# Kernel optimization log

Hardware: AMD Instinct MI355X
Metric: run time of the kernel (lower is better)

Reference implementation:

```python
import jax, jax.numpy as jnp
import numpy as np

B, S, H1, H2, D4, LAT, DD1, DD2, K = 8192, 4096, 196, 10, 1024, 32, 1024, 2048, 21

def _knn_mask(rng, rows, cols, k):
    # disjoint-group style mask: each column has exactly k ones (as produced by knnLayer's non-overlap grouping)
    m = np.zeros((rows, cols), dtype=np.float32)
    order = np.argsort(rng.random((rows, cols)), axis=0)[:k]  # [k, cols]
    m[order, np.arange(cols)[None, :]] = 1.0
    return m

def _glorot(rng, shape):
    lim = np.sqrt(6.0 / (shape[0] + shape[1]))
    return (rng.uniform(-lim, lim, size=shape)).astype(np.float32)

def setup_inputs() -> dict:
    rng = np.random.default_rng(0)
    key = jax.random.key(0)
    x = jax.random.uniform(key, (B, S), dtype=jnp.float32)
    inp = {
        'x': x,
        'C1': jnp.asarray(_knn_mask(rng, S, H1, K)),
        'W1': jnp.asarray(_glorot(rng, (S, H1))),
        'b1': jnp.zeros((H1,), jnp.float32),
        'C2': jnp.asarray(_knn_mask(rng, H1, H2, K)),
        'W2': jnp.asarray(_glorot(rng, (H1, H2))),
        'b2': jnp.zeros((H2,), jnp.float32),
        'W3': jnp.asarray(_glorot(rng, (H2, D4))),
        'b3': jnp.zeros((D4,), jnp.float32),
        'W4': jnp.asarray(_glorot(rng, (D4, LAT))),
        'b4': jnp.zeros((LAT,), jnp.float32),
        'Wd1': jnp.asarray(_glorot(rng, (LAT, DD1))),
        'bd1': jnp.zeros((DD1,), jnp.float32),
        'Wd2': jnp.asarray(_glorot(rng, (DD1, DD2))),
        'bd2': jnp.zeros((DD2,), jnp.float32),
        'Wd3': jnp.asarray(_glorot(rng, (DD2, S))),
        'bd3': jnp.zeros((S,), jnp.float32),
    }
    return inp

def reference(x, C1, W1, b1, C2, W2, b2, W3, b3, W4, b4, Wd1, bd1, Wd2, bd2, Wd3, bd3):
    # encoder: two masked (CustomConnected) layers + two dense layers
    h = jax.nn.relu(x @ (W1 * C1) + b1)            # [B, H1]
    h = jax.nn.relu(h @ (W2 * C2) + b2)            # [B, H2]
    h = jax.nn.relu(h @ W3 + b3)                    # [B, S/4]
    z = jax.nn.relu(h @ W4 + b4)                    # [B, latent]
    # decoder: relu, relu, sigmoid
    d = jax.nn.relu(z @ Wd1 + bd1)                  # [B, S/4]
    d = jax.nn.relu(d @ Wd2 + bd2)                  # [B, S/2]
    out = jax.nn.sigmoid(d @ Wd3 + bd3)             # [B, S]
    return out
```

## Files before the change

kernel.cpp:

```cpp
#include <hip/hip_runtime.h>
#include <hip/hip_fp8.h>
#include <cstdint>
#include <cstddef>

typedef __attribute__((ext_vector_type(4))) float f32x4;
typedef __attribute__((ext_vector_type(8))) int i32x8;

#define DEVINL __device__ __forceinline__

DEVINL unsigned short f2bf(float f){
  union { float f; unsigned u; } v; v.f = f;
  unsigned r = v.u + 0x7fffu + ((v.u >> 16) & 1u);
  return (unsigned short)(r >> 16);
}
DEVINL float bf2f(unsigned short h){
  union { unsigned u; float f; } v; v.u = ((unsigned)h) << 16;
  return v.f;
}
DEVINL unsigned char f2fp8(float f){
  __hip_fp8_e4m3 t(f);
  return (unsigned char)t.__x;
}
DEVINL void gload_lds16(const void* g, void* l){
  __builtin_amdgcn_global_load_lds((const __attribute__((address_space(1))) void*)g,
                                   (__attribute__((address_space(3))) void*)l, 16, 0, 0);
}

#define ACT_SCALE 64.0f
#define W_SCALE   16.0f
#define E8M0_ACT  121
#define E8M0_W    123

__global__ __launch_bounds__(256) void transpose_fp8(
    const float* __restrict__ W, unsigned char* __restrict__ Wt, int K, int N)
{
  __shared__ unsigned char tile[32][33];
  int k0 = blockIdx.x * 32, n0 = blockIdx.y * 32;
  int tx = threadIdx.x & 31, ty = threadIdx.x >> 5;
  #pragma unroll
  for (int i = 0; i < 4; ++i) {
    int k = k0 + ty + 8*i, n = n0 + tx;
    tile[ty + 8*i][tx] = f2fp8(W[(size_t)k*N + n] * W_SCALE);
  }
  __syncthreads();
  #pragma unroll
  for (int i = 0; i < 4; ++i) {
    int n = n0 + ty + 8*i, k = k0 + tx;
    Wt[(size_t)n*K + k] = tile[tx][ty + 8*i];
  }
}

__global__ __launch_bounds__(256) void build_sparse(
    const float* __restrict__ C1, const float* __restrict__ W1,
    unsigned* __restrict__ packed)
{
  const int j = blockIdx.x;
  const int w = threadIdx.x >> 6, l = threadIdx.x & 63;
  __shared__ int wcnt[4], wbase[4];
  int cnt = 0;
  #pragma unroll 4
  for (int it = 0; it < 16; ++it) {
    int k = w*1024 + it*64 + l;
    float c = C1[(size_t)k*196 + j];
    unsigned long long m = __ballot(c != 0.f);
    cnt += (int)__popcll(m);
  }
  if (l == 0) wcnt[w] = cnt;
  __syncthreads();
  if (threadIdx.x < 21) packed[j*21 + threadIdx.x] = 0;
  if (threadIdx.x == 0) {
    int b = 0;
    #pragma unroll
    for (int i = 0; i < 4; ++i) { wbase[i] = b; b += wcnt[i]; }
  }
  __syncthreads();
  int base = wbase[w];
  #pragma unroll 4
  for (int it = 0; it < 16; ++it) {
    int k = w*1024 + it*64 + l;
    float c = C1[(size_t)k*196 + j];
    unsigned long long m = __ballot(c != 0.f);
    if (c != 0.f) {
      int pos = base + (int)__popcll(m & ((1ull << l) - 1ull));
      if (pos < 21)
        packed[j*21 + pos] = ((unsigned)k << 16)
                           | (unsigned)f2bf(W1[(size_t)k*196 + j] * c);
    }
    base += (int)__popcll(m);
  }
}

__global__ __launch_bounds__(256) void layer1_sparse(
    const float* __restrict__ x, const unsigned* __restrict__ packed,
    const float* __restrict__ b1, unsigned short* __restrict__ h1)
{
  __shared__ float xs[2*4096];
  const int t = threadIdx.x;
  const long m0 = (long)blockIdx.x * 2;
  const float4* src = (const float4*)(x + m0*4096);
  #pragma unroll
  for (int i = 0; i < 8; ++i) ((float4*)xs)[t + i*256] = src[t + i*256];
  __syncthreads();
  for (int e = t; e < 2*196; e += 256) {
    int row = (e >= 196) ? 1 : 0;
    int col = e - row*196;
    const float* xr = xs + row*4096;
    float acc = b1[col];
    #pragma unroll
    for (int i = 0; i < 21; ++i) {
      unsigned p = packed[col*21 + i];
      acc += xr[p >> 16] * bf2f((unsigned short)(p & 0xffffu));
    }
    h1[(m0 + row)*256 + col] = f2bf(fmaxf(acc, 0.f));
  }
}

template<int ACT>
__global__ __launch_bounds__(256) void gemm_fp8(
    const unsigned char* __restrict__ A, const unsigned char* __restrict__ Bt,
    const float* __restrict__ bias, void* __restrict__ Cptr, int K, int ldC)
{
  constexpr int BM = 128, BN = 128, BK = 128;
  constexpr int HM = 64, HN = 64, FM = 4, FN = 4;
  __shared__ __align__(16) unsigned char smem[32768];
  unsigned char* As = smem;
  unsigned char* Bs = smem + 16384;
  const int tid  = threadIdx.x;
  const int lane = tid & 63;
  const int w    = tid >> 6;
  const int wm = w & 1, wn = w >> 1;
  const int q = lane >> 4, l16 = lane & 15;
  const long m0 = (long)blockIdx.x * BM;
  const long n0 = (long)blockIdx.y * BN;

  f32x4 acc[FM][FN] = {};

  for (int k0 = 0; k0 < K; k0 += BK) {
    #pragma unroll
    for (int it = 0; it < 4; ++it) {
      int seg = tid + it*256;
      int row = seg >> 3;
      int g   = (5*(seg & 7) + 3*row) & 7;
      gload_lds16(A + (m0 + row)*(long)K + k0 + g*16, As + seg*16);
    }
    #pragma unroll
    for (int it = 0; it < 4; ++it) {
      int seg = tid + it*256;
      int row = seg >> 3;
      int g   = (5*(seg & 7) + 3*row) & 7;
      gload_lds16(Bt + (n0 + row)*(long)K + k0 + g*16, Bs + seg*16);
    }
    __syncthreads();

    i32x8 a[FM], b[FN];
    #pragma unroll
    for (int i = 0; i < FM; ++i) {
      int r = wm*HM + i*16 + l16;
      const uint4* p = (const uint4*)(As + r*BK);
      int c0 = (2*q + r) & 7;
      union { uint4 v[2]; i32x8 f; } u;
      u.v[0] = p[c0];
      u.v[1] = p[(c0 + 5) & 7];
      a[i] = u.f;
    }
    #pragma unroll
    for (int j = 0; j < FN; ++j) {
      int r = wn*HN + j*16 + l16;
      const uint4* p = (const uint4*)(Bs + r*BK);
      int c0 = (2*q + r) & 7;
      union { uint4 v[2]; i32x8 f; } u;
      u.v[0] = p[c0];
      u.v[1] = p[(c0 + 5) & 7];
      b[j] = u.f;
    }
    #pragma unroll
    for (int i = 0; i < FM; ++i)
      #pragma unroll
      for (int j = 0; j < FN; ++j)
        acc[i][j] = __builtin_amdgcn_mfma_scale_f32_16x16x128_f8f6f4(
            a[i], b[j], acc[i][j], 0, 0, 0, E8M0_ACT, 0, E8M0_W);
    __syncthreads();
  }

  if constexpr (ACT == 0) {
    #pragma unroll
    for (int j = 0; j < FN; ++j) {
      int cl = wn*HN + j*16 + l16;
      float bv = bias[n0 + cl];
      #pragma unroll
      for (int i = 0; i < FM; ++i) {
        #pragma unroll
        for (int r = 0; r < 4; ++r) {
          int rl = wm*HM + i*16 + q*4 + r;
          smem[rl*144 + cl] = f2fp8(fmaxf(acc[i][j][r] + bv, 0.f) * ACT_SCALE);
        }
      }
    }
    __syncthreads();
    unsigned char* C = (unsigned char*)Cptr;
    #pragma unroll
    for (int it = 0; it < 4; ++it) {
      int seg = tid + it*256;
      int row = seg >> 3;
      *(uint4*)(C + (m0 + row)*(long)ldC + n0 + (seg & 7)*16) =
          *(const uint4*)(smem + row*144 + (seg & 7)*16);
    }
  } else {
    float* C = (float*)Cptr;
    #pragma unroll
    for (int j = 0; j < FN; ++j) {
      long col = n0 + wn*HN + j*16 + l16;
      float bv = bias[col];
      #pragma unroll
      for (int i = 0; i < FM; ++i) {
        #pragma unroll
        for (int r = 0; r < 4; ++r) {
          long row = m0 + wm*HM + i*16 + q*4 + r;
          float v = acc[i][j][r] + bv;
          C[row*(long)ldC + col] = 1.f / (1.f + __expf(-v));
        }
      }
    }
  }
}

__global__ __launch_bounds__(256) void layer2345(
    const unsigned short* __restrict__ h1,
    const float* __restrict__ W2, const float* __restrict__ C2, const float* __restrict__ b2,
    const float* __restrict__ W3, const float* __restrict__ b3,
    const float* __restrict__ W4, const float* __restrict__ b4,
    const float* __restrict__ Wd1, const float* __restrict__ bd1,
    unsigned char* __restrict__ d1)
{
  __shared__ float h1s[4][200];
  __shared__ float h2s[4][10];
  __shared__ float h3s[4][1024];
  __shared__ float part[8][128];
  __shared__ float zs[4][32];
  const int t = threadIdx.x;
  const int w = t >> 6, l = t & 63;
  const long m0 = (long)blockIdx.x * 4;

  for (int e = t; e < 4*196; e += 256) {
    int row = e / 196, col = e - row*196;
    h1s[row][col] = bf2f(h1[(m0 + row)*256 + col]);
  }
  __syncthreads();

  {
    float acc[10];
    #pragma unroll
    for (int n = 0; n < 10; ++n) acc[n] = 0.f;
    #pragma unroll
    for (int it = 0; it < 4; ++it) {
      int k = l + it*64;
      if (k < 196) {
        float a = h1s[w][k];
        #pragma unroll
        for (int n = 0; n < 10; ++n) acc[n] += a * W2[k*10 + n] * C2[k*10 + n];
      }
    }
    #pragma unroll
    for (int off = 32; off > 0; off >>= 1) {
      #pragma unroll
      for (int n = 0; n < 10; ++n) acc[n] += __shfl_down(acc[n], off, 64);
    }
    if (l < 10) h2s[w][l] = fmaxf(acc[l] + b2[l], 0.f);
  }
  __syncthreads();

  #pragma unroll
  for (int jj = 0; jj < 4; ++jj) {
    int n = w*256 + jj*64 + l;
    float a0 = b3[n], a1 = a0, a2 = a0, a3 = a0;
    #pragma unroll
    for (int k = 0; k < 10; ++k) {
      float wv = W3[k*1024 + n];
      a0 += h2s[0][k]*wv; a1 += h2s[1][k]*wv;
      a2 += h2s[2][k]*wv; a3 += h2s[3][k]*wv;
    }
    h3s[0][n] = fmaxf(a0, 0.f); h3s[1][n] = fmaxf(a1, 0.f);
    h3s[2][n] = fmaxf(a2, 0.f); h3s[3][n] = fmaxf(a3, 0.f);
  }
  __syncthreads();

  {
    int n = t & 31, kg = t >> 5;
    float a0 = 0.f, a1 = 0.f, a2 = 0.f, a3 = 0.f;
    for (int k = kg*128; k < kg*128 + 128; ++k) {
      float wv = W4[k*32 + n];
      a0 += h3s[0][k]*wv; a1 += h3s[1][k]*wv;
      a2 += h3s[2][k]*wv; a3 += h3s[3][k]*wv;
    }
    part[kg][0*32 + n] = a0; part[kg][1*32 + n] = a1;
    part[kg][2*32 + n] = a2; part[kg][3*32 + n] = a3;
  }
  __syncthreads();
  if (t < 128) {
    float s = 0.f;
    #pragma unroll
    for (int kg = 0; kg < 8; ++kg) s += part[kg][t];
    zs[t >> 5][t & 31] = fmaxf(s + b4[t & 31], 0.f);
  }
  __syncthreads();

  #pragma unroll
  for (int jj = 0; jj < 4; ++jj) {
    int n = w*256 + jj*64 + l;
    float a0 = bd1[n], a1 = a0, a2 = a0, a3 = a0;
    #pragma unroll
    for (int k = 0; k < 32; ++k) {
      float wv = Wd1[k*1024 + n];
      a0 += zs[0][k]*wv; a1 += zs[1][k]*wv;
      a2 += zs[2][k]*wv; a3 += zs[3][k]*wv;
    }
    d1[(m0 + 0)*1024 + n] = f2fp8(fmaxf(a0, 0.f) * ACT_SCALE);
    d1[(m0 + 1)*1024 + n] = f2fp8(fmaxf(a1, 0.f) * ACT_SCALE);
    d1[(m0 + 2)*1024 + n] = f2fp8(fmaxf(a2, 0.f) * ACT_SCALE);
    d1[(m0 + 3)*1024 + n] = f2fp8(fmaxf(a3, 0.f) * ACT_SCALE);
  }
}

extern "C" void kernel_launch(void* const* d_in, const int* in_sizes, int n_in,
                              void* d_out, int out_size, void* d_ws, size_t ws_size,
                              hipStream_t stream)
{
  (void)in_sizes; (void)n_in; (void)out_size; (void)ws_size;
  const float* x   = (const float*)d_in[0];
  const float* C1  = (const float*)d_in[1];
  const float* W1  = (const float*)d_in[2];
  const float* b1  = (const float*)d_in[3];
  const float* C2  = (const float*)d_in[4];
  const float* W2  = (const float*)d_in[5];
  const float* b2  = (const float*)d_in[6];
  const float* W3  = (const float*)d_in[7];
  const float* b3  = (const float*)d_in[8];
  const float* W4  = (const float*)d_in[9];
  const float* b4  = (const float*)d_in[10];
  const float* Wd1 = (const float*)d_in[11];
  const float* bd1 = (const float*)d_in[12];
  const float* Wd2 = (const float*)d_in[13];
  const float* bd2 = (const float*)d_in[14];
  const float* Wd3 = (const float*)d_in[15];
  const float* bd3 = (const float*)d_in[16];
  float* out = (float*)d_out;

  char* ws = (char*)d_ws;
  size_t off = 0;
  auto alloc = [&](size_t bytes) -> void* {
    void* p = ws + off; off += (bytes + 255) & ~(size_t)255; return p;
  };
  unsigned char* Wt2 = (unsigned char*)alloc((size_t)2048*1024);
  unsigned char* Wt3 = (unsigned char*)alloc((size_t)4096*2048);
  unsigned*      pk  = (unsigned*)     alloc((size_t)196*21*4);
  unsigned short* h1 = (unsigned short*)alloc((size_t)8192*256*2);
  unsigned char*  d1 = (unsigned char*) alloc((size_t)8192*1024);
  unsigned char*  d2 = (unsigned char*) alloc((size_t)8192*2048);

  build_sparse<<<dim3(196), 256, 0, stream>>>(C1, W1, pk);
  transpose_fp8<<<dim3(1024/32, 2048/32), 256, 0, stream>>>(Wd2, Wt2, 1024, 2048);
  transpose_fp8<<<dim3(2048/32, 4096/32), 256, 0, stream>>>(Wd3, Wt3, 2048, 4096);

  layer1_sparse<<<dim3(8192/2), 256, 0, stream>>>(x, pk, b1, h1);
  layer2345<<<dim3(8192/4), 256, 0, stream>>>(h1, W2, C2, b2, W3, b3, W4, b4,
                                              Wd1, bd1, d1);
  gemm_fp8<0><<<dim3(8192/128, 2048/128), 256, 0, stream>>>(
      d1, Wt2, bd2, d2, 1024, 2048);
  gemm_fp8<1><<<dim3(8192/128, 4096/128), 256, 0, stream>>>(
      d2, Wt3, bd3, out, 2048, 4096);
}
```

Before: 464.5 us.

## Rewrite FP8 GEMM as 256x256 double-buffered 8-wave kernel with phased prefetch

```diff
diff --git a/kernel.cpp b/kernel.cpp
--- a/kernel.cpp
+++ b/kernel.cpp
@@ -115,107 +115,174 @@
   }
 }
 
+
+#define MXMFMA(va, vb, c) __builtin_amdgcn_mfma_scale_f32_16x16x128_f8f6f4( \
+    (va), (vb), (c), 0, 0, 0, E8M0_ACT, 0, E8M0_W)
+
+#define MFMA8(I, va0, va1) \
+  acc[(I)][0]   = MXMFMA(va0, b0, acc[(I)][0]); \
+  acc[(I)][1]   = MXMFMA(va0, b1, acc[(I)][1]); \
+  acc[(I)][2]   = MXMFMA(va0, b2, acc[(I)][2]); \
+  acc[(I)][3]   = MXMFMA(va0, b3, acc[(I)][3]); \
+  acc[(I)+1][0] = MXMFMA(va1, b0, acc[(I)+1][0]); \
+  acc[(I)+1][1] = MXMFMA(va1, b1, acc[(I)+1][1]); \
+  acc[(I)+1][2] = MXMFMA(va1, b2, acc[(I)+1][2]); \
+  acc[(I)+1][3] = MXMFMA(va1, b3, acc[(I)+1][3]);
+
 template<int ACT>
-__global__ __launch_bounds__(256) void gemm_fp8(
+__global__ __launch_bounds__(512, 2) void gemm_fp8_8ph(
     const unsigned char* __restrict__ A, const unsigned char* __restrict__ Bt,
     const float* __restrict__ bias, void* __restrict__ Cptr, int K, int ldC)
 {
-  constexpr int BM = 128, BN = 128, BK = 128;
-  constexpr int HM = 64, HN = 64, FM = 4, FN = 4;
-  __shared__ __align__(16) unsigned char smem[32768];
-  unsigned char* As = smem;
-  unsigned char* Bs = smem + 16384;
+  constexpr int BM = 256, BN = 256;
+  extern __shared__ unsigned char sm[];
   const int tid  = threadIdx.x;
   const int lane = tid & 63;
   const int w    = tid >> 6;
-  const int wm = w & 1, wn = w >> 1;
+  const int wm = w >> 2, wn = w & 3;
   const int q = lane >> 4, l16 = lane & 15;
   const long m0 = (long)blockIdx.x * BM;
   const long n0 = (long)blockIdx.y * BN;
 
-  f32x4 acc[FM][FN] = {};
-
-  for (int k0 = 0; k0 < K; k0 += BK) {
-    #pragma unroll
-    for (int it = 0; it < 4; ++it) {
-      int seg = tid + it*256;
-      int row = seg >> 3;
-      int g   = (5*(seg & 7) + 3*row) & 7;
-      gload_lds16(A + (m0 + row)*(long)K + k0 + g*16, As + seg*16);
-    }
-    #pragma unroll
-    for (int it = 0; it < 4; ++it) {
-      int seg = tid + it*256;
-      int row = seg >> 3;
-      int g   = (5*(seg & 7) + 3*row) & 7;
-      gload_lds16(Bt + (n0 + row)*(long)K + k0 + g*16, Bs + seg*16);
-    }
+  unsigned char* Ac = sm;
+  unsigned char* Bc = sm + 32768;
+  unsigned char* An = sm + 65536;
+  unsigned char* Bn = sm + 98304;
+
+  f32x4 acc[8][4] = {};
+  const int NT = K >> 7;
+
+  auto stageA = [&](unsigned char* Ld, int qr, int kk) {
+    int seg  = qr*512 + tid;
+    int rblk = seg >> 7, ci = seg & 127;
+    int h = ci >> 6, rem = ci & 63;
+    int qq = rem >> 4, rloc = rem & 15;
+    int r = rblk*16 + rloc, c = qq*2 + h;
+    gload_lds16(A + (m0 + r)*(long)K + kk + c*16, Ld + seg*16);
+  };
+  auto stageB = [&](unsigned char* Ld, int qr, int kk) {
+    int seg  = qr*512 + tid;
+    int rblk = seg >> 7, ci = seg & 127;
+    int h = ci >> 6, rem = ci & 63;
+    int qq = rem >> 4, rloc = rem & 15;
+    int r = rblk*16 + rloc, c = qq*2 + h;
+    gload_lds16(Bt + (n0 + r)*(long)K + kk + c*16, Ld + seg*16);
+  };
+  auto rdfrag = [&](const unsigned char* Ld, int rblk) -> i32x8 {
+    union { uint4 v[2]; i32x8 f; } u;
+    const unsigned char* p = Ld + rblk*2048 + lane*16;
+    u.v[0] = *(const uint4*)p;
+    u.v[1] = *(const uint4*)(p + 1024);
+    return u.f;
+  };
+
+  #pragma unroll
+  for (int qr = 0; qr < 4; ++qr) stageA(Ac, qr, 0);
+  #pragma unroll
+  for (int qr = 0; qr < 4; ++qr) stageB(Bc, qr, 0);
+  asm volatile("s_waitcnt vmcnt(0)" ::: "memory");
+  __builtin_amdgcn_s_barrier();
+
+  for (int kt = 0; kt < NT; ++kt) {
+    const bool haveNext = (kt + 1 < NT);
+    const int kk = (kt + 1) << 7;
+    i32x8 b0, b1, b2, b3;
+
+    if (haveNext) { stageB(Bn, 0, kk); stageB(Bn, 1, kk); }
+    b0 = rdfrag(Bc, wn*4 + 0); b1 = rdfrag(Bc, wn*4 + 1);
+    b2 = rdfrag(Bc, wn*4 + 2); b3 = rdfrag(Bc, wn*4 + 3);
+    {
+      i32x8 a0 = rdfrag(Ac, wm*8 + 0), a1 = rdfrag(Ac, wm*8 + 1);
+      __builtin_amdgcn_s_barrier();
+      asm volatile("s_waitcnt lgkmcnt(0)" ::: "memory");
+      __builtin_amdgcn_sched_barrier(0);
+      __builtin_amdgcn_s_setprio(1);
+      MFMA8(0, a0, a1)
+      __builtin_amdgcn_s_setprio(0);
+      __builtin_amdgcn_s_barrier();
+    }
+
+    if (haveNext) { stageB(Bn, 2, kk); stageB(Bn, 3, kk); }
+    {
+      i32x8 a0 = rdfrag(Ac, wm*8 + 2), a1 = rdfrag(Ac, wm*8 + 3);
+      if (haveNext) { asm volatile("s_waitcnt vmcnt(4)" ::: "memory"); }
+      else          { asm volatile("s_waitcnt vmcnt(0)" ::: "memory"); }
+      __builtin_amdgcn_s_barrier();
+      asm volatile("s_waitcnt lgkmcnt(0)" ::: "memory");
+      __builtin_amdgcn_sched_barrier(0);
+      __builtin_amdgcn_s_setprio(1);
+      MFMA8(2, a0, a1)
+      __builtin_amdgcn_s_setprio(0);
+      __builtin_amdgcn_s_barrier();
+    }
+
+    if (haveNext) { stageA(An, 0, kk); stageA(An, 2, kk); }
+    {
+      i32x8 a0 = rdfrag(Ac, wm*8 + 4), a1 = rdfrag(Ac, wm*8 + 5);
+      __builtin_amdgcn_s_barrier();
+      asm volatile("s_waitcnt lgkmcnt(0)" ::: "memory");
+      __builtin_amdgcn_sched_barrier(0);
+      __builtin_amdgcn_s_setprio(1);
+      MFMA8(4, a0, a1)
+      __builtin_amdgcn_s_setprio(0);
+      __builtin_amdgcn_s_barrier();
+    }
+
+    if (haveNext) { stageA(An, 1, kk); stageA(An, 3, kk); }
+    {
+      i32x8 a0 = rdfrag(Ac, wm*8 + 6), a1 = rdfrag(Ac, wm*8 + 7);
+      if (haveNext) { asm volatile("s_waitcnt vmcnt(2)" ::: "memory"); }
+      else          { asm volatile("s_waitcnt vmcnt(0)" ::: "memory"); }
+      __builtin_amdgcn_s_barrier();
+      asm volatile("s_waitcnt lgkmcnt(0)" ::: "memory");
+      __builtin_amdgcn_sched_barrier(0);
+      __builtin_amdgcn_s_setprio(1);
+      MFMA8(6, a0, a1)
+      __builtin_amdgcn_s_setprio(0);
+      __builtin_amdgcn_s_barrier();
+    }
+
+    unsigned char* t;
+    t = Ac; Ac = An; An = t;
+    t = Bc; Bc = Bn; Bn = t;
+  }
+
+  if constexpr (ACT == 0) {
     __syncthreads();
-
-    i32x8 a[FM], b[FN];
-    #pragma unroll
-    for (int i = 0; i < FM; ++i) {
-      int r = wm*HM + i*16 + l16;
-      const uint4* p = (const uint4*)(As + r*BK);
-      int c0 = (2*q + r) & 7;
-      union { uint4 v[2]; i32x8 f; } u;
-      u.v[0] = p[c0];
-      u.v[1] = p[(c0 + 5) & 7];
-      a[i] = u.f;
-    }
-    #pragma unroll
-    for (int j = 0; j < FN; ++j) {
-      int r = wn*HN + j*16 + l16;
-      const uint4* p = (const uint4*)(Bs + r*BK);
-      int c0 = (2*q + r) & 7;
-      union { uint4 v[2]; i32x8 f; } u;
-      u.v[0] = p[c0];
-      u.v[1] = p[(c0 + 5) & 7];
-      b[j] = u.f;
-    }
-    #pragma unroll
-    for (int i = 0; i < FM; ++i)
-      #pragma unroll
-      for (int j = 0; j < FN; ++j)
-        acc[i][j] = __builtin_amdgcn_mfma_scale_f32_16x16x128_f8f6f4(
-            a[i], b[j], acc[i][j], 0, 0, 0, E8M0_ACT, 0, E8M0_W);
-    __syncthreads();
-  }
-
-  if constexpr (ACT == 0) {
-    #pragma unroll
-    for (int j = 0; j < FN; ++j) {
-      int cl = wn*HN + j*16 + l16;
+    unsigned char* eb = sm;
+    #pragma unroll
+    for (int j = 0; j < 4; ++j) {
+      int cl = wn*64 + j*16 + l16;
       float bv = bias[n0 + cl];
       #pragma unroll
-      for (int i = 0; i < FM; ++i) {
+      for (int i = 0; i < 8; ++i) {
         #pragma unroll
         for (int r = 0; r < 4; ++r) {
-          int rl = wm*HM + i*16 + q*4 + r;
-          smem[rl*144 + cl] = f2fp8(fmaxf(acc[i][j][r] + bv, 0.f) * ACT_SCALE);
+          int rl = wm*128 + i*16 + q*4 + r;
+          eb[rl*272 + cl] = f2fp8(fmaxf(acc[i][j][r] + bv, 0.f) * ACT_SCALE);
         }
       }
     }
     __syncthreads();
     unsigned char* C = (unsigned char*)Cptr;
     #pragma unroll
-    for (int it = 0; it < 4; ++it) {
-      int seg = tid + it*256;
-      int row = seg >> 3;
-      *(uint4*)(C + (m0 + row)*(long)ldC + n0 + (seg & 7)*16) =
-          *(const uint4*)(smem + row*144 + (seg & 7)*16);
+    for (int it = 0; it < 8; ++it) {
+      int seg = tid + it*512;
+      int row = seg >> 4, ch = seg & 15;
+      *(uint4*)(C + (m0 + row)*(long)ldC + n0 + ch*16) =
+          *(const uint4*)(eb + row*272 + ch*16);
     }
   } else {
     float* C = (float*)Cptr;
     #pragma unroll
-    for (int j = 0; j < FN; ++j) {
-      long col = n0 + wn*HN + j*16 + l16;
+    for (int j = 0; j < 4; ++j) {
+      long col = n0 + wn*64 + j*16 + l16;
       float bv = bias[col];
       #pragma unroll
-      for (int i = 0; i < FM; ++i) {
+      for (int i = 0; i < 8; ++i) {
         #pragma unroll
         for (int r = 0; r < 4; ++r) {
-          long row = m0 + wm*HM + i*16 + q*4 + r;
+          long row = m0 + wm*128 + i*16 + q*4 + r;
           float v = acc[i][j][r] + bv;
           C[row*(long)ldC + col] = 1.f / (1.f + __expf(-v));
         }
@@ -357,6 +424,15 @@
   unsigned char*  d1 = (unsigned char*) alloc((size_t)8192*1024);
   unsigned char*  d2 = (unsigned char*) alloc((size_t)8192*2048);
 
+  static int attr_set = 0;
+  if (!attr_set) {
+    hipFuncSetAttribute((const void*)gemm_fp8_8ph<0>,
+                        hipFuncAttributeMaxDynamicSharedMemorySize, 131072);
+    hipFuncSetAttribute((const void*)gemm_fp8_8ph<1>,
+                        hipFuncAttributeMaxDynamicSharedMemorySize, 131072);
+    attr_set = 1;
+  }
+
   build_sparse<<<dim3(196), 256, 0, stream>>>(C1, W1, pk);
   transpose_fp8<<<dim3(1024/32, 2048/32), 256, 0, stream>>>(Wd2, Wt2, 1024, 2048);
   transpose_fp8<<<dim3(2048/32, 4096/32), 256, 0, stream>>>(Wd3, Wt3, 2048, 4096);
@@ -364,8 +440,8 @@
   layer1_sparse<<<dim3(8192/2), 256, 0, stream>>>(x, pk, b1, h1);
   layer2345<<<dim3(8192/4), 256, 0, stream>>>(h1, W2, C2, b2, W3, b3, W4, b4,
                                               Wd1, bd1, d1);
-  gemm_fp8<0><<<dim3(8192/128, 2048/128), 256, 0, stream>>>(
+  gemm_fp8_8ph<0><<<dim3(8192/256, 2048/256), 512, 131072, stream>>>(
       d1, Wt2, bd2, d2, 1024, 2048);
-  gemm_fp8<1><<<dim3(8192/128, 4096/128), 256, 0, stream>>>(
+  gemm_fp8_8ph<1><<<dim3(8192/256, 4096/256), 512, 131072, stream>>>(
       d2, Wt3, bd3, out, 2048, 4096);
 }
```

New measurement: 561.0 us. 20.8% more time.
